# Kernel tuning notes

Hardware: AMD Instinct MI355X
Metric: run time of the kernel (lower is better)

## Reference

```python
import jax, jax.numpy as jnp
import numpy as np

EMPTY, TRUE, FALSE = 0.0, 1.0, 2.0  # MemoryVal ternary encoding

B = 2048          # batch
IN_BITS = 4096    # raw input bits
N_IN, N_ST, N_OUT = 2048, 1024, 1024
K = 14            # bits (connections) per neuron -> memory_size = 2**K
M = 2 ** K


def setup_inputs() -> dict:
    key = jax.random.key(0)
    ks = jax.random.split(key, 8)
    return {
        "input_bits": jax.random.randint(ks[0], (B, IN_BITS), 0, 2, dtype=jnp.int32),
        "state_bits": jax.random.randint(ks[1], (B, N_ST), 0, 2, dtype=jnp.int32),
        "in_conn": jax.random.randint(ks[2], (N_IN, K), 0, IN_BITS, dtype=jnp.int32),
        "in_mem": jax.random.randint(ks[3], (N_IN, M), 0, 3).astype(jnp.float32),
        "st_conn": jax.random.randint(ks[4], (N_ST, K), 0, N_IN + N_ST, dtype=jnp.int32),
        "st_mem": jax.random.randint(ks[5], (N_ST, M), 0, 3).astype(jnp.float32),
        "out_conn": jax.random.randint(ks[6], (N_OUT, K), 0, N_IN + N_ST, dtype=jnp.int32),
        "out_mem": jax.random.randint(ks[7], (N_OUT, M), 0, 3).astype(jnp.float32),
    }


def _ram_layer(bits, conn, mem):
    """bits: [B, T] 0/1; conn: [N, K] indices into T; mem: [N, 2**K] ternary."""
    k = conn.shape[1]
    g = bits[:, conn].astype(jnp.int32)                      # [B, N, K] gathered local bits
    w = (2 ** jnp.arange(k - 1, -1, -1)).astype(jnp.int32)   # MSB-first packing (matches _get_desired_bits)
    addr = jnp.sum(g * w, axis=-1)                           # [B, N] memory addresses
    vals = mem[jnp.arange(mem.shape[0])[None, :], addr]      # [B, N] per-neuron LUT lookup
    return jnp.where(vals == TRUE, 1.0, 0.0).astype(jnp.float32)  # neuron fires iff TRUE


def reference(input_bits, state_bits, in_conn, in_mem, st_conn, st_mem, out_conn, out_mem):
    h_in = _ram_layer(input_bits, in_conn, in_mem)                          # [B, N_IN]
    s_inp = jnp.concatenate([h_in, state_bits.astype(h_in.dtype)], axis=1)  # [B, N_IN+N_ST]
    s_out = _ram_layer(s_inp, st_conn, st_mem)                              # [B, N_ST]
    o_inp = jnp.concatenate([h_in, s_out], axis=1)                          # [B, N_IN+N_ST]
    return _ram_layer(o_inp, out_conn, out_mem)                             # [B, N_OUT]
```

## Files before the change

### kernel.cpp

```cpp
#include <hip/hip_runtime.h>
#include <stdint.h>

#define BATCH   2048
#define IN_BITS 4096
#define N_IN    2048
#define N_ST    1024
#define N_OUT   1024
#define KBITS   14
#define MW      512
#define SROW    96

__global__ __launch_bounds__(256) void pack_i32(const int* __restrict__ src,
                                                uint32_t* __restrict__ dst,
                                                int total_words, int wshift,
                                                int dst_stride, int dst_off) {
    int t = blockIdx.x * 256 + threadIdx.x;
    if (t >= total_words) return;
    int r = t >> wshift;
    int c = t & ((1 << wshift) - 1);
    const int4* p = (const int4*)(src + ((long)r << (wshift + 5)) + (c << 5));
    uint32_t w = 0;
#pragma unroll
    for (int j = 0; j < 8; j++) {
        int4 v = p[j];
        w |= (uint32_t)(v.x == 1) << (4 * j + 0);
        w |= (uint32_t)(v.y == 1) << (4 * j + 1);
        w |= (uint32_t)(v.z == 1) << (4 * j + 2);
        w |= (uint32_t)(v.w == 1) << (4 * j + 3);
    }
    dst[(long)r * dst_stride + dst_off + c] = w;
}

__global__ __launch_bounds__(256) void pack_f32(const float* __restrict__ src,
                                                uint32_t* __restrict__ dst,
                                                int total_words) {
    int t = blockIdx.x * 256 + threadIdx.x;
    if (t >= total_words) return;
    const float4* p = (const float4*)(src + (long)t * 32);
    uint32_t w = 0;
#pragma unroll
    for (int j = 0; j < 8; j++) {
        float4 v = p[j];
        w |= (uint32_t)(v.x == 1.0f) << (4 * j + 0);
        w |= (uint32_t)(v.y == 1.0f) << (4 * j + 1);
        w |= (uint32_t)(v.z == 1.0f) << (4 * j + 2);
        w |= (uint32_t)(v.w == 1.0f) << (4 * j + 3);
    }
    dst[t] = w;
}

template <int SRCW, int BCHUNK, int MODE>
__global__ __launch_bounds__(256) void ram_layer(const uint32_t* __restrict__ src,
                                                 const int* __restrict__ conn,
                                                 const uint32_t* __restrict__ memp,
                                                 uint32_t* __restrict__ dst0,
                                                 uint32_t* __restrict__ dst1,
                                                 float* __restrict__ fout) {
    __shared__ uint32_t lds[BCHUNK * SRCW];
    const int tid = threadIdx.x;
    const int b0 = blockIdx.y * BCHUNK;

    {
        const uint4* g = (const uint4*)(src + (long)b0 * SRCW);
        uint4* l = (uint4*)lds;
        constexpr int NV = BCHUNK * SRCW / 4;
        for (int i = tid; i < NV; i += 256) l[i] = g[i];
    }
    __syncthreads();

    const int n = blockIdx.x * 256 + tid;
    int wd[KBITS], sh[KBITS];
#pragma unroll
    for (int k = 0; k < KBITS; k++) {
        int idx = conn[n * KBITS + k];
        wd[k] = idx >> 5;
        sh[k] = idx & 31;
    }
    const uint32_t* mrow = memp + (long)n * MW;
    const int lane = tid & 63;
    const int nbase = blockIdx.x * 256 + (tid & ~63);

#pragma unroll 4
    for (int bb = 0; bb < BCHUNK; ++bb) {
        const uint32_t* row = lds + bb * SRCW;
        uint32_t addr = 0;
#pragma unroll
        for (int k = 0; k < KBITS; k++)
            addr = (addr << 1) | ((row[wd[k]] >> sh[k]) & 1u);
        uint32_t bit = (mrow[addr >> 5] >> (addr & 31)) & 1u;
        const int b = b0 + bb;
        if (MODE == 2) {
            fout[(long)b * N_OUT + n] = (float)bit;
        } else {
            unsigned long long m = __ballot(bit != 0);
            if (lane == 0) {
                if (MODE == 0) {
                    *(unsigned long long*)(dst0 + (long)b * SROW + (nbase >> 5)) = m;
                    *(unsigned long long*)(dst1 + (long)b * SROW + (nbase >> 5)) = m;
                } else {
                    *(unsigned long long*)(dst0 + (long)b * SROW + 64 + (nbase >> 5)) = m;
                }
            }
        }
    }
}

extern "C" void kernel_launch(void* const* d_in, const int* in_sizes, int n_in,
                              void* d_out, int out_size, void* d_ws, size_t ws_size,
                              hipStream_t stream) {
    const int*   input_bits = (const int*)d_in[0];
    const int*   state_bits = (const int*)d_in[1];
    const int*   in_conn    = (const int*)d_in[2];
    const float* in_mem     = (const float*)d_in[3];
    const int*   st_conn    = (const int*)d_in[4];
    const float* st_mem     = (const float*)d_in[5];
    const int*   out_conn   = (const int*)d_in[6];
    const float* out_mem    = (const float*)d_in[7];
    float*       out        = (float*)d_out;

    char* ws = (char*)d_ws;
    uint32_t* bits1 = (uint32_t*)(ws);
    uint32_t* buf_s = (uint32_t*)(ws + 1048576);
    uint32_t* buf_o = (uint32_t*)(ws + 1048576 + 786432);
    uint32_t* im_p  = (uint32_t*)(ws + 1048576 + 2 * 786432);
    uint32_t* sm_p  = (uint32_t*)(ws + 1048576 + 2 * 786432 + 4194304);
    uint32_t* om_p  = (uint32_t*)(ws + 1048576 + 2 * 786432 + 4194304 + 2097152);

    pack_i32<<<(BATCH * 128 + 255) / 256, 256, 0, stream>>>(input_bits, bits1,
                                                            BATCH * 128, 7, 128, 0);
    pack_i32<<<(BATCH * 32 + 255) / 256, 256, 0, stream>>>(state_bits, buf_s,
                                                           BATCH * 32, 5, SROW, 64);
    pack_f32<<<(N_IN * MW + 255) / 256, 256, 0, stream>>>(in_mem, im_p, N_IN * MW);
    pack_f32<<<(N_ST * MW + 255) / 256, 256, 0, stream>>>(st_mem, sm_p, N_ST * MW);
    pack_f32<<<(N_OUT * MW + 255) / 256, 256, 0, stream>>>(out_mem, om_p, N_OUT * MW);

    ram_layer<128, 16, 0><<<dim3(N_IN / 256, BATCH / 16), 256, 0, stream>>>(
        bits1, in_conn, im_p, buf_s, buf_o, nullptr);
    ram_layer<SROW, 8, 1><<<dim3(N_ST / 256, BATCH / 8), 256, 0, stream>>>(
        buf_s, st_conn, sm_p, buf_o, nullptr, nullptr);
    ram_layer<SROW, 8, 2><<<dim3(N_OUT / 256, BATCH / 8), 256, 0, stream>>>(
        buf_o, out_conn, om_p, nullptr, nullptr, out);
}
```

Baseline: 366.4 us.

## Transpose RAM layer mapping to lanes-per-batch with ballot packing and bit transpose

Replaces the packing kernels with coalesced ballot-based packers and merges the three memory-table packs into one launch. The RAM layer now maps each lane to a batch row and loops over neurons. Connection indices are wave-uniform, so they can be scalar loads, and each lane reads its own padded LDS row. Per-neuron ballots are transposed with a 6-step shuffle network so each lane holds one batch row's packed bits. Output is written as packed bits and expanded to floats in a separate kernel, which trades one extra launch for fewer scattered stores. The input and state layers now share a single combined buffer.

```diff
diff --git a/kernel.cpp b/kernel.cpp
--- a/kernel.cpp
+++ b/kernel.cpp
@@ -8,101 +8,172 @@
 #define N_OUT   1024
 #define KBITS   14
 #define MW      512
-#define SROW    96
-
-__global__ __launch_bounds__(256) void pack_i32(const int* __restrict__ src,
-                                                uint32_t* __restrict__ dst,
-                                                int total_words, int wshift,
-                                                int dst_stride, int dst_off) {
-    int t = blockIdx.x * 256 + threadIdx.x;
-    if (t >= total_words) return;
-    int r = t >> wshift;
-    int c = t & ((1 << wshift) - 1);
-    const int4* p = (const int4*)(src + ((long)r << (wshift + 5)) + (c << 5));
-    uint32_t w = 0;
-#pragma unroll
-    for (int j = 0; j < 8; j++) {
-        int4 v = p[j];
-        w |= (uint32_t)(v.x == 1) << (4 * j + 0);
-        w |= (uint32_t)(v.y == 1) << (4 * j + 1);
-        w |= (uint32_t)(v.z == 1) << (4 * j + 2);
-        w |= (uint32_t)(v.w == 1) << (4 * j + 3);
-    }
-    dst[(long)r * dst_stride + dst_off + c] = w;
-}
-
-__global__ __launch_bounds__(256) void pack_f32(const float* __restrict__ src,
-                                                uint32_t* __restrict__ dst,
-                                                int total_words) {
-    int t = blockIdx.x * 256 + threadIdx.x;
-    if (t >= total_words) return;
-    const float4* p = (const float4*)(src + (long)t * 32);
-    uint32_t w = 0;
-#pragma unroll
-    for (int j = 0; j < 8; j++) {
-        float4 v = p[j];
-        w |= (uint32_t)(v.x == 1.0f) << (4 * j + 0);
-        w |= (uint32_t)(v.y == 1.0f) << (4 * j + 1);
-        w |= (uint32_t)(v.z == 1.0f) << (4 * j + 2);
-        w |= (uint32_t)(v.w == 1.0f) << (4 * j + 3);
-    }
-    dst[t] = w;
-}
-
-template <int SRCW, int BCHUNK, int MODE>
+
+#define BROW 128
+#define PAD  129
+
+#define IM_F 33554432L
+#define SM_F 16777216L
+#define OM_F 16777216L
+
+__global__ __launch_bounds__(256) void pack_mem(const float* __restrict__ im,
+                                                const float* __restrict__ sm,
+                                                const float* __restrict__ om,
+                                                uint32_t* __restrict__ dst) {
+    int wid = (blockIdx.x * 256 + threadIdx.x) >> 6;
+    int lane = threadIdx.x & 63;
+    long f0 = (long)wid << 10;
+    const float* s;
+    long base;
+    if (f0 < IM_F)              { s = im; base = f0; }
+    else if (f0 < IM_F + SM_F)  { s = sm; base = f0 - IM_F; }
+    else                        { s = om; base = f0 - (IM_F + SM_F); }
+    unsigned long long m[16];
+#pragma unroll
+    for (int j = 0; j < 16; j++)
+        m[j] = __ballot(s[base + j * 64 + lane] == 1.0f);
+    if (lane == 0) {
+        uint4* o = (uint4*)(dst + (f0 >> 5));
+#pragma unroll
+        for (int j = 0; j < 8; j++) {
+            uint4 q;
+            q.x = (uint32_t)m[2 * j];
+            q.y = (uint32_t)(m[2 * j] >> 32);
+            q.z = (uint32_t)m[2 * j + 1];
+            q.w = (uint32_t)(m[2 * j + 1] >> 32);
+            o[j] = q;
+        }
+    }
+}
+
+__global__ __launch_bounds__(256) void pack_in(const int* __restrict__ src,
+                                               uint32_t* __restrict__ dst) {
+    int wid = (blockIdx.x * 256 + threadIdx.x) >> 6;
+    int lane = threadIdx.x & 63;
+    long f0 = (long)wid << 10;
+    unsigned long long m[16];
+#pragma unroll
+    for (int j = 0; j < 16; j++)
+        m[j] = __ballot(src[f0 + j * 64 + lane] == 1);
+    if (lane == 0) {
+        uint4* o = (uint4*)(dst + (f0 >> 5));
+#pragma unroll
+        for (int j = 0; j < 8; j++) {
+            uint4 q;
+            q.x = (uint32_t)m[2 * j];
+            q.y = (uint32_t)(m[2 * j] >> 32);
+            q.z = (uint32_t)m[2 * j + 1];
+            q.w = (uint32_t)(m[2 * j + 1] >> 32);
+            o[j] = q;
+        }
+    }
+}
+
+__global__ __launch_bounds__(256) void pack_st(const int* __restrict__ src,
+                                               uint32_t* __restrict__ buf) {
+    int wid = (blockIdx.x * 256 + threadIdx.x) >> 6;
+    int lane = threadIdx.x & 63;
+    long f0 = (long)wid << 10;
+    unsigned long long m[16];
+#pragma unroll
+    for (int j = 0; j < 16; j++)
+        m[j] = __ballot(src[f0 + j * 64 + lane] == 1);
+    if (lane == 0) {
+        uint4* o = (uint4*)(buf + (long)wid * BROW + 64);
+#pragma unroll
+        for (int j = 0; j < 8; j++) {
+            uint4 q;
+            q.x = (uint32_t)m[2 * j];
+            q.y = (uint32_t)(m[2 * j] >> 32);
+            q.z = (uint32_t)m[2 * j + 1];
+            q.w = (uint32_t)(m[2 * j + 1] >> 32);
+            o[j] = q;
+        }
+    }
+}
+
+template <int NW, int MODE>
 __global__ __launch_bounds__(256) void ram_layer(const uint32_t* __restrict__ src,
                                                  const int* __restrict__ conn,
                                                  const uint32_t* __restrict__ memp,
-                                                 uint32_t* __restrict__ dst0,
-                                                 uint32_t* __restrict__ dst1,
-                                                 float* __restrict__ fout) {
-    __shared__ uint32_t lds[BCHUNK * SRCW];
+                                                 uint32_t* __restrict__ dst) {
+    __shared__ uint32_t lds[64 * PAD];
     const int tid = threadIdx.x;
-    const int b0 = blockIdx.y * BCHUNK;
+    const int b0 = blockIdx.y * 64;
 
     {
-        const uint4* g = (const uint4*)(src + (long)b0 * SRCW);
-        uint4* l = (uint4*)lds;
-        constexpr int NV = BCHUNK * SRCW / 4;
-        for (int i = tid; i < NV; i += 256) l[i] = g[i];
+        const uint4* g = (const uint4*)(src + (long)b0 * BROW);
+        for (int v = tid; v < 64 * BROW / 4; v += 256) {
+            uint4 d = g[v];
+            int row = v >> 5;
+            int col = (v & 31) * 4;
+            uint32_t* p = lds + row * PAD + col;
+            p[0] = d.x; p[1] = d.y; p[2] = d.z; p[3] = d.w;
+        }
     }
     __syncthreads();
 
-    const int n = blockIdx.x * 256 + tid;
-    int wd[KBITS], sh[KBITS];
-#pragma unroll
-    for (int k = 0; k < KBITS; k++) {
-        int idx = conn[n * KBITS + k];
-        wd[k] = idx >> 5;
-        sh[k] = idx & 31;
-    }
-    const uint32_t* mrow = memp + (long)n * MW;
     const int lane = tid & 63;
-    const int nbase = blockIdx.x * 256 + (tid & ~63);
-
-#pragma unroll 4
-    for (int bb = 0; bb < BCHUNK; ++bb) {
-        const uint32_t* row = lds + bb * SRCW;
+    const int wv = __builtin_amdgcn_readfirstlane(tid >> 6);
+    const int n0 = blockIdx.x * (4 * NW) + wv * NW;
+    const uint32_t* myrow = lds + lane * PAD;
+
+    unsigned long long msk = 0;
+#pragma unroll 2
+    for (int i = 0; i < NW; ++i) {
+        const int n = n0 + i;
+        const int* c = conn + n * KBITS;
         uint32_t addr = 0;
 #pragma unroll
-        for (int k = 0; k < KBITS; k++)
-            addr = (addr << 1) | ((row[wd[k]] >> sh[k]) & 1u);
-        uint32_t bit = (mrow[addr >> 5] >> (addr & 31)) & 1u;
-        const int b = b0 + bb;
-        if (MODE == 2) {
-            fout[(long)b * N_OUT + n] = (float)bit;
-        } else {
-            unsigned long long m = __ballot(bit != 0);
-            if (lane == 0) {
-                if (MODE == 0) {
-                    *(unsigned long long*)(dst0 + (long)b * SROW + (nbase >> 5)) = m;
-                    *(unsigned long long*)(dst1 + (long)b * SROW + (nbase >> 5)) = m;
-                } else {
-                    *(unsigned long long*)(dst0 + (long)b * SROW + 64 + (nbase >> 5)) = m;
-                }
-            }
-        }
-    }
+        for (int k = 0; k < KBITS; k++) {
+            int idx = c[k];
+            int wd = idx >> 5;
+            if (MODE == 2 && idx >= 2048) wd += 32;
+            addr = (addr << 1) | ((myrow[wd] >> (idx & 31)) & 1u);
+        }
+        uint32_t v = memp[(long)n * MW + (addr >> 5)];
+        unsigned long long m = __ballot(((v >> (addr & 31)) & 1u) != 0);
+        msk = (lane == i) ? m : msk;
+    }
+
+    unsigned long long x = msk;
+#define TSTEP(S, M)                                                         \
+    {                                                                       \
+        unsigned long long t =                                              \
+            (unsigned long long)__shfl_xor((long long)x, S, 64);            \
+        x = (lane & S) ? ((x & ~(M)) | ((t & ~(M)) >> S))                   \
+                       : ((x & (M)) | ((t & (M)) << S));                    \
+    }
+    TSTEP(32, 0x00000000ffffffffULL)
+    TSTEP(16, 0x0000ffff0000ffffULL)
+    TSTEP(8,  0x00ff00ff00ff00ffULL)
+    TSTEP(4,  0x0f0f0f0f0f0f0f0fULL)
+    TSTEP(2,  0x3333333333333333ULL)
+    TSTEP(1,  0x5555555555555555ULL)
+#undef TSTEP
+
+    if (MODE == 0) {
+        *(uint32_t*)(dst + (long)(b0 + lane) * BROW + (n0 >> 5)) = (uint32_t)x;
+    } else if (MODE == 1) {
+        ((uint16_t*)(dst + (long)(b0 + lane) * BROW + 96))[n0 >> 4] = (uint16_t)x;
+    } else {
+        ((uint16_t*)(dst + (long)(b0 + lane) * 32))[n0 >> 4] = (uint16_t)x;
+    }
+}
+
+__global__ __launch_bounds__(256) void expand_out(const uint32_t* __restrict__ pout,
+                                                  float4* __restrict__ out) {
+    int t = blockIdx.x * 256 + threadIdx.x;
+    int b = t >> 8;
+    int c4 = (t & 255) * 4;
+    uint32_t w = pout[b * 32 + (c4 >> 5)];
+    int sh = c4 & 31;
+    float4 f;
+    f.x = (float)((w >> (sh + 0)) & 1u);
+    f.y = (float)((w >> (sh + 1)) & 1u);
+    f.z = (float)((w >> (sh + 2)) & 1u);
+    f.w = (float)((w >> (sh + 3)) & 1u);
+    out[t] = f;
 }
 
 extern "C" void kernel_launch(void* const* d_in, const int* in_sizes, int n_in,
@@ -120,24 +191,20 @@
 
     char* ws = (char*)d_ws;
     uint32_t* bits1 = (uint32_t*)(ws);
-    uint32_t* buf_s = (uint32_t*)(ws + 1048576);
-    uint32_t* buf_o = (uint32_t*)(ws + 1048576 + 786432);
-    uint32_t* im_p  = (uint32_t*)(ws + 1048576 + 2 * 786432);
-    uint32_t* sm_p  = (uint32_t*)(ws + 1048576 + 2 * 786432 + 4194304);
-    uint32_t* om_p  = (uint32_t*)(ws + 1048576 + 2 * 786432 + 4194304 + 2097152);
-
-    pack_i32<<<(BATCH * 128 + 255) / 256, 256, 0, stream>>>(input_bits, bits1,
-                                                            BATCH * 128, 7, 128, 0);
-    pack_i32<<<(BATCH * 32 + 255) / 256, 256, 0, stream>>>(state_bits, buf_s,
-                                                           BATCH * 32, 5, SROW, 64);
-    pack_f32<<<(N_IN * MW + 255) / 256, 256, 0, stream>>>(in_mem, im_p, N_IN * MW);
-    pack_f32<<<(N_ST * MW + 255) / 256, 256, 0, stream>>>(st_mem, sm_p, N_ST * MW);
-    pack_f32<<<(N_OUT * MW + 255) / 256, 256, 0, stream>>>(out_mem, om_p, N_OUT * MW);
-
-    ram_layer<128, 16, 0><<<dim3(N_IN / 256, BATCH / 16), 256, 0, stream>>>(
-        bits1, in_conn, im_p, buf_s, buf_o, nullptr);
-    ram_layer<SROW, 8, 1><<<dim3(N_ST / 256, BATCH / 8), 256, 0, stream>>>(
-        buf_s, st_conn, sm_p, buf_o, nullptr, nullptr);
-    ram_layer<SROW, 8, 2><<<dim3(N_OUT / 256, BATCH / 8), 256, 0, stream>>>(
-        buf_o, out_conn, om_p, nullptr, nullptr, out);
-}
+    uint32_t* buf   = (uint32_t*)(ws + 1048576);
+    uint32_t* pout  = (uint32_t*)(ws + 2097152);
+    uint32_t* tbl   = (uint32_t*)(ws + 2359296);
+    uint32_t* im_p  = tbl;
+    uint32_t* sm_p  = tbl + 1048576;
+    uint32_t* om_p  = tbl + 1572864;
+
+    pack_in<<<2048, 256, 0, stream>>>(input_bits, bits1);
+    pack_st<<<512, 256, 0, stream>>>(state_bits, buf);
+    pack_mem<<<16384, 256, 0, stream>>>(in_mem, st_mem, out_mem, tbl);
+
+    ram_layer<32, 0><<<dim3(16, 32), 256, 0, stream>>>(bits1, in_conn, im_p, buf);
+    ram_layer<16, 1><<<dim3(16, 32), 256, 0, stream>>>(buf, st_conn, sm_p, buf);
+    ram_layer<16, 2><<<dim3(16, 32), 256, 0, stream>>>(buf, out_conn, om_p, pout);
+
+    expand_out<<<2048, 256, 0, stream>>>(pout, (float4*)out);
+}
```

After: 370.9 us. About the same (+1.2%).
